# Kernel tuning notes

Measured on AMD Instinct MI355X. Metric: run time of the kernel, lower is better.

The kernel has to match this reference:

```python
import jax, jax.numpy as jnp
import numpy as np

BATCH = 32
DIM = 768


def _packed_pool_indices(seq_lens_np, kernel_size, stride):
    """Host-side (static) index construction for packed ragged avg-pool.

    Returns gather indices [total_y, K] into the packed x and a validity mask,
    mirroring the Triton forward_pooling_kernel's masked window loads.
    """
    sl = np.asarray(seq_lens_np, np.int64)
    x_cu = np.concatenate([np.zeros(1, np.int64), np.cumsum(sl)])
    # compute_output_shape: ceil_div(max(0, L - K), S) + 1, 0 if L == 0
    y_lens = np.where(sl == 0, 0, -(-np.maximum(sl - kernel_size, 0) // stride) + 1)
    y_cu = np.concatenate([np.zeros(1, np.int64), np.cumsum(y_lens)])
    total_y = int(y_cu[-1])
    b = np.repeat(np.arange(len(sl)), y_lens)                 # batch id per output token
    j = np.arange(total_y) - np.repeat(y_cu[:-1], y_lens)    # local output position
    pos = j[:, None] * stride + np.arange(kernel_size)[None, :]  # [total_y, K] input pos
    lens_b = sl[b][:, None]
    valid = pos < lens_b                                       # mask = idx_x_seq < x_seq_len
    idx = x_cu[b][:, None] + np.minimum(pos, np.maximum(lens_b - 1, 0))
    return jnp.asarray(idx, jnp.int32), jnp.asarray(valid)


def setup_inputs() -> dict:
    key = jax.random.key(0)
    seq_lens = (1024 + 97 * np.arange(BATCH)).astype(np.int32)  # ragged, total = 80880
    total_tokens = int(seq_lens.sum())
    x = jax.random.normal(key, (total_tokens, DIM), dtype=jnp.float32)
    return {"x": x, "seq_lens": jnp.asarray(seq_lens), "kernel_size": 2, "stride": 2}


def reference(x, seq_lens, kernel_size, stride):
    # seq_lens are structural constants (define the ragged layout)
    idx, valid = _packed_pool_indices(np.asarray(jax.device_get(seq_lens)), kernel_size, stride)
    gathered = x[idx]                            # [total_y, K, D]
    m = valid.astype(x.dtype)[:, :, None]        # [total_y, K, 1]
    # masked average over the kernel window: norm = 1 / count of valid taps
    return (gathered * m).sum(axis=1) / m.sum(axis=1)
```

## Files before the change

kernel.cpp:

```cpp
#include <hip/hip_runtime.h>


#define DIM 768
#define D4  (DIM / 4)

typedef float vfloat4 __attribute__((ext_vector_type(4)));

__global__ __launch_bounds__(D4) void packed_avgpool_rows(
    const float4* __restrict__ x,
    const int*    __restrict__ seq_lens,
    const int*    __restrict__ kptr,
    const int*    __restrict__ sptr,
    float4*       __restrict__ out,
    int batch)
{
    __shared__ int s_base;
    __shared__ int s_p0;
    __shared__ int s_L;
    __shared__ int s_K;

    const int row = blockIdx.x;

    if (threadIdx.x < 64) {
        const int lane = threadIdx.x;
        const int K = kptr[0];
        const int S = sptr[0];
        int L = (lane < batch) ? seq_lens[lane] : 0;
        int over = (L > K) ? (L - K) : 0;
        int yl   = (L == 0) ? 0 : (over + S - 1) / S + 1;

        int xs = L, ys = yl;
        #pragma unroll
        for (int off = 1; off < 64; off <<= 1) {
            int xv = __shfl_up(xs, off);
            int yv = __shfl_up(ys, off);
            if (lane >= off) { xs += xv; ys += yv; }
        }

        unsigned long long bal = __ballot(ys <= row);
        int b   = (int)__popcll(bal);
        int xcu = (b == 0) ? 0 : __shfl(xs, b - 1);
        int ycu = (b == 0) ? 0 : __shfl(ys, b - 1);
        int Lb  = __shfl(L, b);
        if (lane == 0) {
            s_base = xcu;
            s_p0   = (row - ycu) * S;
            s_L    = Lb;
            s_K    = K;
        }
    }
    __syncthreads();

    const int K    = s_K;
    const int L    = s_L;
    const int p0   = s_p0;
    const int base = s_base;
    const int col  = threadIdx.x;

    float4 acc = make_float4(0.f, 0.f, 0.f, 0.f);
    float  cnt = 0.f;
    for (int k = 0; k < K; ++k) {
        int   pos  = p0 + k;
        int   cpos = (pos < L) ? pos : (L - 1);
        float m    = (pos < L) ? 1.f : 0.f;
        float4 v = x[(long long)(base + cpos) * D4 + col];
        acc.x += m * v.x; acc.y += m * v.y; acc.z += m * v.z; acc.w += m * v.w;
        cnt   += m;
    }
    const float inv = 1.0f / cnt;
    vfloat4 r = { acc.x * inv, acc.y * inv, acc.z * inv, acc.w * inv };
    __builtin_nontemporal_store(
        r, (vfloat4*)&out[(long long)row * D4 + col]);
}

extern "C" void kernel_launch(void* const* d_in, const int* in_sizes, int n_in,
                              void* d_out, int out_size, void* d_ws, size_t ws_size,
                              hipStream_t stream) {
    const float4* x        = (const float4*)d_in[0];
    const int*    seq_lens = (const int*)d_in[1];
    const int*    kptr     = (const int*)d_in[2];
    const int*    sptr     = (const int*)d_in[3];
    float4*       out      = (float4*)d_out;

    const int batch   = in_sizes[1];
    const int total_y = out_size / DIM;

    packed_avgpool_rows<<<total_y, D4, 0, stream>>>(
        x, seq_lens, kptr, sptr, out, batch);
}
```

Baseline: 373.2 us.

## Process eight output rows per block and specialize the kernel-size-2 path

Each block now handles eight output rows, so the per-block prefix scan over sequence lengths is amortized across more work and there are fewer, larger blocks. A fast path for K==2 issues both loads for a row without a loop, allowing more loads in flight per thread. Index math switches from 64-bit to 32-bit, which fits the sizes used here but could overflow for larger inputs. Tail blocks mask out-of-range rows by setting their length to zero.

```diff
diff --git a/kernel.cpp b/kernel.cpp
--- a/kernel.cpp
+++ b/kernel.cpp
@@ -1,8 +1,9 @@
 #include <hip/hip_runtime.h>
 
 
-#define DIM 768
-#define D4  (DIM / 4)
+#define DIM  768
+#define D4   (DIM / 4)
+#define ROWS 8
 
 typedef float vfloat4 __attribute__((ext_vector_type(4)));
 
@@ -12,14 +13,14 @@
     const int*    __restrict__ kptr,
     const int*    __restrict__ sptr,
     float4*       __restrict__ out,
-    int batch)
+    int batch, int total_y)
 {
-    __shared__ int s_base;
-    __shared__ int s_p0;
-    __shared__ int s_L;
+    __shared__ int s_base[ROWS];
+    __shared__ int s_p0[ROWS];
+    __shared__ int s_L[ROWS];
     __shared__ int s_K;
 
-    const int row = blockIdx.x;
+    const int row0 = blockIdx.x * ROWS;
 
     if (threadIdx.x < 64) {
         const int lane = threadIdx.x;
@@ -37,40 +38,76 @@
             if (lane >= off) { xs += xv; ys += yv; }
         }
 
-        unsigned long long bal = __ballot(ys <= row);
-        int b   = (int)__popcll(bal);
-        int xcu = (b == 0) ? 0 : __shfl(xs, b - 1);
-        int ycu = (b == 0) ? 0 : __shfl(ys, b - 1);
-        int Lb  = __shfl(L, b);
-        if (lane == 0) {
-            s_base = xcu;
-            s_p0   = (row - ycu) * S;
-            s_L    = Lb;
-            s_K    = K;
+        if (lane == 0) s_K = K;
+
+        #pragma unroll
+        for (int r = 0; r < ROWS; ++r) {
+            const int row = row0 + r;
+            unsigned long long bal = __ballot(ys <= row);
+            int b   = (int)__popcll(bal);
+            int xcu = (b == 0) ? 0 : __shfl(xs, b - 1);
+            int ycu = (b == 0) ? 0 : __shfl(ys, b - 1);
+            int Lb  = __shfl(L, b & 63);
+            if (lane == 0) {
+                s_base[r] = xcu;
+                s_p0[r]   = (row - ycu) * S;
+                s_L[r]    = (row < total_y) ? Lb : 0;
+            }
         }
     }
     __syncthreads();
 
-    const int K    = s_K;
-    const int L    = s_L;
-    const int p0   = s_p0;
-    const int base = s_base;
-    const int col  = threadIdx.x;
+    const int K   = s_K;
+    const int col = threadIdx.x;
 
-    float4 acc = make_float4(0.f, 0.f, 0.f, 0.f);
-    float  cnt = 0.f;
-    for (int k = 0; k < K; ++k) {
-        int   pos  = p0 + k;
-        int   cpos = (pos < L) ? pos : (L - 1);
-        float m    = (pos < L) ? 1.f : 0.f;
-        float4 v = x[(long long)(base + cpos) * D4 + col];
-        acc.x += m * v.x; acc.y += m * v.y; acc.z += m * v.z; acc.w += m * v.w;
-        cnt   += m;
+    if (K == 2) {
+        #pragma unroll
+        for (int r = 0; r < ROWS; ++r) {
+            const int L = s_L[r];
+            if (L == 0) continue;
+            const int base = s_base[r];
+            const int p0   = s_p0[r];
+
+            const int  p1    = p0 + 1;
+            const int  c1    = (p1 < L) ? p1 : (L - 1);
+            const float m1   = (p1 < L) ? 1.f : 0.f;
+
+            float4 v0 = x[(base + p0) * D4 + col];
+            float4 v1 = x[(base + c1) * D4 + col];
+
+            const float inv = 1.0f / (1.0f + m1);
+            vfloat4 rv = { (v0.x + m1 * v1.x) * inv,
+                           (v0.y + m1 * v1.y) * inv,
+                           (v0.z + m1 * v1.z) * inv,
+                           (v0.w + m1 * v1.w) * inv };
+            __builtin_nontemporal_store(
+                rv, (vfloat4*)&out[(row0 + r) * D4 + col]);
+        }
+    } else {
+        #pragma unroll
+        for (int r = 0; r < ROWS; ++r) {
+            const int L = s_L[r];
+            if (L == 0) continue;
+            const int base = s_base[r];
+            const int p0   = s_p0[r];
+
+            float4 acc = make_float4(0.f, 0.f, 0.f, 0.f);
+            float  cnt = 0.f;
+            for (int k = 0; k < K; ++k) {
+                int   pos  = p0 + k;
+                int   cpos = (pos < L) ? pos : (L - 1);
+                float m    = (pos < L) ? 1.f : 0.f;
+                float4 v = x[(base + cpos) * D4 + col];
+                acc.x += m * v.x; acc.y += m * v.y;
+                acc.z += m * v.z; acc.w += m * v.w;
+                cnt   += m;
+            }
+            const float inv = 1.0f / cnt;
+            vfloat4 rv = { acc.x * inv, acc.y * inv, acc.z * inv, acc.w * inv };
+            __builtin_nontemporal_store(
+                rv, (vfloat4*)&out[(row0 + r) * D4 + col]);
+        }
     }
-    const float inv = 1.0f / cnt;
-    vfloat4 r = { acc.x * inv, acc.y * inv, acc.z * inv, acc.w * inv };
-    __builtin_nontemporal_store(
-        r, (vfloat4*)&out[(long long)row * D4 + col]);
 }
 
 extern "C" void kernel_launch(void* const* d_in, const int* in_sizes, int n_in,
@@ -84,7 +121,8 @@
 
     const int batch   = in_sizes[1];
     const int total_y = out_size / DIM;
+    const int nblocks = (total_y + ROWS - 1) / ROWS;
 
-    packed_avgpool_rows<<<total_y, D4, 0, stream>>>(
-        x, seq_lens, kptr, sptr, out, batch);
+    packed_avgpool_rows<<<nblocks, D4, 0, stream>>>(
+        x, seq_lens, kptr, sptr, out, batch, total_y);
 }
```

New measurement: 385.7 us. +3.3%, slower.

## Process output rows per wavefront with a grid-stride loop and a K==2 fast path

Applied to the files above, without the earlier changes.

Replaces the one-block-per-row launch, where one 192-thread block runs a scan and a syncthreads per row, with a persistent grid of 4-wave blocks. Each wave computes the prefix scan of sequence lengths once, then strides over rows, doing the row lookup through ballot and shuffle with no shared memory or block barrier. A K==2 specialisation issues all six vector loads up front, and loads are marked nontemporal. This cuts per-row launch and synchronisation overhead and raises memory-level parallelism, at the cost of capping the grid at 2048 blocks.

```diff
diff --git a/kernel.cpp b/kernel.cpp
--- a/kernel.cpp
+++ b/kernel.cpp
@@ -3,88 +3,115 @@
 
 #define DIM 768
 #define D4  (DIM / 4)
+#define WPB 4
+#define BLOCK (WPB * 64)
 
 typedef float vfloat4 __attribute__((ext_vector_type(4)));
 
-__global__ __launch_bounds__(D4) void packed_avgpool_rows(
-    const float4* __restrict__ x,
-    const int*    __restrict__ seq_lens,
-    const int*    __restrict__ kptr,
-    const int*    __restrict__ sptr,
-    float4*       __restrict__ out,
-    int batch)
+__global__ __launch_bounds__(BLOCK) void packed_avgpool_waves(
+    const vfloat4* __restrict__ x,
+    const int*     __restrict__ seq_lens,
+    const int*     __restrict__ kptr,
+    const int*     __restrict__ sptr,
+    vfloat4*       __restrict__ out,
+    int batch, int total_y, int nwaves)
 {
-    __shared__ int s_base;
-    __shared__ int s_p0;
-    __shared__ int s_L;
-    __shared__ int s_K;
+    const int lane = threadIdx.x & 63;
+    const int wid  = blockIdx.x * WPB + (threadIdx.x >> 6);
 
-    const int row = blockIdx.x;
+    const int K = kptr[0];
+    const int S = sptr[0];
 
-    if (threadIdx.x < 64) {
-        const int lane = threadIdx.x;
-        const int K = kptr[0];
-        const int S = sptr[0];
-        int L = (lane < batch) ? seq_lens[lane] : 0;
-        int over = (L > K) ? (L - K) : 0;
-        int yl   = (L == 0) ? 0 : (over + S - 1) / S + 1;
+    int L    = (lane < batch) ? seq_lens[lane] : 0;
+    int over = (L > K) ? (L - K) : 0;
+    int yl   = (L == 0) ? 0 : (over + S - 1) / S + 1;
 
-        int xs = L, ys = yl;
-        #pragma unroll
-        for (int off = 1; off < 64; off <<= 1) {
-            int xv = __shfl_up(xs, off);
-            int yv = __shfl_up(ys, off);
-            if (lane >= off) { xs += xv; ys += yv; }
+    int xs = L, ys = yl;
+    #pragma unroll
+    for (int off = 1; off < 64; off <<= 1) {
+        int xv = __shfl_up(xs, off);
+        int yv = __shfl_up(ys, off);
+        if (lane >= off) { xs += xv; ys += yv; }
+    }
+
+    if (K == 2) {
+        for (int row = wid; row < total_y; row += nwaves) {
+            unsigned long long bal = __ballot(ys <= row);
+            int b   = (int)__popcll(bal) & 63;
+            int ib  = (b > 0) ? (b - 1) : 0;
+            int xcu = __shfl(xs, ib);  if (b == 0) xcu = 0;
+            int ycu = __shfl(ys, ib);  if (b == 0) ycu = 0;
+            int Lb  = __shfl(L, b);
+
+            const int   p0 = (row - ycu) * S;
+            const int   p1 = p0 + 1;
+            const int   c1 = (p1 < Lb) ? p1 : (Lb - 1);
+            const float m1 = (p1 < Lb) ? 1.f : 0.f;
+
+            const vfloat4* r0 = x + (long long)(xcu + p0) * D4;
+            const vfloat4* r1 = x + (long long)(xcu + c1) * D4;
+
+            vfloat4 a0 = __builtin_nontemporal_load(r0 + lane);
+            vfloat4 a1 = __builtin_nontemporal_load(r0 + lane + 64);
+            vfloat4 a2 = __builtin_nontemporal_load(r0 + lane + 128);
+            vfloat4 b0 = __builtin_nontemporal_load(r1 + lane);
+            vfloat4 b1 = __builtin_nontemporal_load(r1 + lane + 64);
+            vfloat4 b2 = __builtin_nontemporal_load(r1 + lane + 128);
+
+            const float inv = 1.0f / (1.0f + m1);
+            vfloat4* o = out + (long long)row * D4;
+            __builtin_nontemporal_store((a0 + m1 * b0) * inv, o + lane);
+            __builtin_nontemporal_store((a1 + m1 * b1) * inv, o + lane + 64);
+            __builtin_nontemporal_store((a2 + m1 * b2) * inv, o + lane + 128);
         }
+    } else {
+        for (int row = wid; row < total_y; row += nwaves) {
+            unsigned long long bal = __ballot(ys <= row);
+            int b   = (int)__popcll(bal) & 63;
+            int ib  = (b > 0) ? (b - 1) : 0;
+            int xcu = __shfl(xs, ib);  if (b == 0) xcu = 0;
+            int ycu = __shfl(ys, ib);  if (b == 0) ycu = 0;
+            int Lb  = __shfl(L, b);
 
-        unsigned long long bal = __ballot(ys <= row);
-        int b   = (int)__popcll(bal);
-        int xcu = (b == 0) ? 0 : __shfl(xs, b - 1);
-        int ycu = (b == 0) ? 0 : __shfl(ys, b - 1);
-        int Lb  = __shfl(L, b);
-        if (lane == 0) {
-            s_base = xcu;
-            s_p0   = (row - ycu) * S;
-            s_L    = Lb;
-            s_K    = K;
+            const int p0 = (row - ycu) * S;
+
+            vfloat4 acc0 = 0.f, acc1 = 0.f, acc2 = 0.f;
+            float   cnt  = 0.f;
+            for (int k = 0; k < K; ++k) {
+                int   pos  = p0 + k;
+                int   cpos = (pos < Lb) ? pos : (Lb - 1);
+                float m    = (pos < Lb) ? 1.f : 0.f;
+                const vfloat4* r = x + (long long)(xcu + cpos) * D4;
+                acc0 += m * __builtin_nontemporal_load(r + lane);
+                acc1 += m * __builtin_nontemporal_load(r + lane + 64);
+                acc2 += m * __builtin_nontemporal_load(r + lane + 128);
+                cnt  += m;
+            }
+            const float inv = 1.0f / cnt;
+            vfloat4* o = out + (long long)row * D4;
+            __builtin_nontemporal_store(acc0 * inv, o + lane);
+            __builtin_nontemporal_store(acc1 * inv, o + lane + 64);
+            __builtin_nontemporal_store(acc2 * inv, o + lane + 128);
         }
     }
-    __syncthreads();
-
-    const int K    = s_K;
-    const int L    = s_L;
-    const int p0   = s_p0;
-    const int base = s_base;
-    const int col  = threadIdx.x;
-
-    float4 acc = make_float4(0.f, 0.f, 0.f, 0.f);
-    float  cnt = 0.f;
-    for (int k = 0; k < K; ++k) {
-        int   pos  = p0 + k;
-        int   cpos = (pos < L) ? pos : (L - 1);
-        float m    = (pos < L) ? 1.f : 0.f;
-        float4 v = x[(long long)(base + cpos) * D4 + col];
-        acc.x += m * v.x; acc.y += m * v.y; acc.z += m * v.z; acc.w += m * v.w;
-        cnt   += m;
-    }
-    const float inv = 1.0f / cnt;
-    vfloat4 r = { acc.x * inv, acc.y * inv, acc.z * inv, acc.w * inv };
-    __builtin_nontemporal_store(
-        r, (vfloat4*)&out[(long long)row * D4 + col]);
 }
 
 extern "C" void kernel_launch(void* const* d_in, const int* in_sizes, int n_in,
                               void* d_out, int out_size, void* d_ws, size_t ws_size,
                               hipStream_t stream) {
-    const float4* x        = (const float4*)d_in[0];
-    const int*    seq_lens = (const int*)d_in[1];
-    const int*    kptr     = (const int*)d_in[2];
-    const int*    sptr     = (const int*)d_in[3];
-    float4*       out      = (float4*)d_out;
+    const vfloat4* x        = (const vfloat4*)d_in[0];
+    const int*     seq_lens = (const int*)d_in[1];
+    const int*     kptr     = (const int*)d_in[2];
+    const int*     sptr     = (const int*)d_in[3];
+    vfloat4*       out      = (vfloat4*)d_out;
 
     const int batch   = in_sizes[1];
     const int total_y = out_size / DIM;
 
-    packed_avgpool_rows<<<total_y, D4, 0, stream>>>(
-        x, seq_lens, kptr, sptr, out, batch);
+    int nblocks = (total_y + WPB - 1) / WPB;
+    if (nblocks > 2048) nblocks = 2048;
+    const int nwaves = nblocks * WPB;
+
+    packed_avgpool_waves<<<nblocks, BLOCK, 0, stream>>>(
+        x, seq_lens, kptr, sptr, out, batch, total_y, nwaves);
 }
```

Result: faster. 354.2 us (-5.1%).
